# Kernel optimization log

Measured on AMD Instinct MI355X. Metric: run time of the kernel, lower is better.

Reference implementation:

```python
import jax, jax.numpy as jnp
import numpy as np

N, E, H, EA, C = 50000, 800000, 128, 32, 4
EPS = 1e-8


def _mlp(x, w1, b1, w2, b2, last_act=False):
    h = jax.nn.silu(x @ w1 + b1)
    o = h @ w2 + b2
    return jax.nn.silu(o) if last_act else o


def _seg_mean(src, idx, n):
    s = jax.ops.segment_sum(src, idx, num_segments=n)
    cnt = jax.ops.segment_sum(jnp.ones((src.shape[0], 1), src.dtype), idx, num_segments=n)
    return s / jnp.maximum(cnt, 1.0)


def setup_inputs() -> dict:
    key = jax.random.key(0)
    ks = jax.random.split(key, 24)

    def lin(k, fan_in, fan_out):
        kw, kb = jax.random.split(k)
        s = 1.0 / np.sqrt(fan_in)
        return (jax.random.uniform(kw, (fan_in, fan_out), jnp.float32, -s, s),
                jax.random.uniform(kb, (fan_out,), jnp.float32, -s, s))

    node_feat = jax.random.normal(ks[0], (N, H), jnp.float32)
    node_pos = jax.random.normal(ks[1], (N, 3), jnp.float32)
    edge_index = jax.random.randint(ks[2], (2, E), 0, N, jnp.int32)
    edge_attr = jax.random.normal(ks[3], (E, EA), jnp.float32)

    fi_w1, fi_b1 = lin(ks[4], H, H)
    fi_w2, fi_b2 = lin(ks[5], H, H)
    msg_in = 2 * H + EA + 4
    msg_w1, msg_b1 = lin(ks[6], msg_in, H)
    msg_w2, msg_b2 = lin(ks[7], H, H)
    co_w1, co_b1 = lin(ks[8], H, H)
    co_w2, co_b2 = lin(ks[9], H, C)
    vf_w1, vf_b1 = lin(ks[10], H, H)
    vf_w2, vf_b2 = lin(ks[11], H, H)

    return dict(node_feat=node_feat, node_pos=node_pos, edge_index=edge_index,
                edge_attr=edge_attr,
                fi_w1=fi_w1, fi_b1=fi_b1, fi_w2=fi_w2, fi_b2=fi_b2,
                msg_w1=msg_w1, msg_b1=msg_b1, msg_w2=msg_w2, msg_b2=msg_b2,
                co_w1=co_w1, co_b1=co_b1, co_w2=co_w2, co_b2=co_b2,
                vf_w1=vf_w1, vf_b1=vf_b1, vf_w2=vf_w2, vf_b2=vf_b2)


def reference(node_feat, node_pos, edge_index, edge_attr,
              fi_w1, fi_b1, fi_w2, fi_b2,
              msg_w1, msg_b1, msg_w2, msg_b2,
              co_w1, co_b1, co_w2, co_b2,
              vf_w1, vf_b1, vf_w2, vf_b2):
    n = node_feat.shape[0]
    # node-level init (mlp_feat_init has last_act=True)
    vn_feat = _mlp(node_feat, fi_w1, fi_b1, fi_w2, fi_b2, last_act=True)
    vn_pos = jnp.tile(node_pos, (1, C))  # [N, 3C]

    row, col = edge_index[0], edge_index[1]
    diff_pos = node_pos[row] - node_pos[col]                      # [E,3]
    nrm = jnp.maximum(jnp.linalg.norm(diff_pos, axis=-1, keepdims=True), EPS)
    diff_vec_norm = diff_pos / nrm                                # [E,3]
    dist_sq = jnp.sum(diff_pos * diff_pos, axis=-1, keepdims=True)
    ip = jnp.tile(dist_sq, (1, 4))                                # [E,4]

    msg = jnp.concatenate([node_feat[row], node_feat[col], edge_attr, ip], axis=1)
    msg = _mlp(msg, msg_w1, msg_b1, msg_w2, msg_b2)               # [E,H]

    # FullyConnectedTensorProduct 1x1o x 1x0e(=1) -> Cx1o reduces to per-channel
    # scaling of the unit vector by the learned weights (path norm factor = 1).
    w_coff = _mlp(msg, co_w1, co_b1, co_w2, co_b2)                # [E,C]
    diff_vec_out = (w_coff[:, :, None] * diff_vec_norm[:, None, :]).reshape(-1, 3 * C)

    agg_feat = _seg_mean(msg, row, n)                             # [N,H]
    agg_vec = _seg_mean(diff_vec_out, row, n)                     # [N,3C]

    vn_feat = vn_feat + _mlp(agg_feat, vf_w1, vf_b1, vf_w2, vf_b2)
    vn_pos = vn_pos + agg_vec
    return (vn_feat, vn_pos)
```

## Files before the change

kernel.cpp:

```cpp
#include <hip/hip_runtime.h>
#include <math.h>

#define N_NODES 50000
#define NTOT    50176
#define NB      196
#define N_EDGES 800000
#define H       128

typedef _Float16 f16x8 __attribute__((ext_vector_type(8)));
typedef _Float16 f16x4 __attribute__((ext_vector_type(4)));
typedef float    f32x4 __attribute__((ext_vector_type(4)));

#define KP1 320
#define KS1 10
#define KS2 4

#define XOFF 0
#define MOFF 0
#define HOFF 40960
#define XSTR 640
#define HSTR 256
#define LDSB 57344

__device__ __forceinline__ float fast_rcp(float x) {
#if __has_builtin(__builtin_amdgcn_rcpf)
    return __builtin_amdgcn_rcpf(x);
#else
    return 1.0f / x;
#endif
}
__device__ __forceinline__ float fast_exp2(float x) {
#if __has_builtin(__builtin_amdgcn_exp2f)
    return __builtin_amdgcn_exp2f(x);
#else
    return exp2f(x);
#endif
}
__device__ __forceinline__ float silu_f(float x) {
    return x * fast_rcp(1.0f + fast_exp2(-1.44269504089f * x));
}

__global__ void pack_w(const float* __restrict__ W, int K, int KP, int NCOL,
                       int CT, _Float16* __restrict__ out) {
    const int idx = blockIdx.x * 256 + threadIdx.x;
    const int KS = KP >> 5;
    if (idx >= CT * 16 * KP) return;
    const int j = idx & 7, l = (idx >> 3) & 63, rem = idx >> 9;
    const int ct = rem / KS, ks = rem % KS;
    const int k = ks * 32 + (l >> 4) * 8 + j;
    const int c = ct * 16 + (l & 15);
    out[idx] = (_Float16)((k < K && c < NCOL) ? W[k * NCOL + c] : 0.0f);
}

__global__ void k_hist(const int* __restrict__ eidx, int* __restrict__ cnt) {
    const int e = blockIdx.x * 256 + threadIdx.x;
    atomicAdd(&cnt[eidx[e]], 1);
}

__global__ void k_scan1(const int* __restrict__ cnt, int* __restrict__ offs,
                        int* __restrict__ bsum) {
    __shared__ int sd[256];
    const int t = threadIdx.x;
    const int idx = blockIdx.x * 256 + t;
    const int v = cnt[idx];
    sd[t] = v;
    __syncthreads();
    for (int off = 1; off < 256; off <<= 1) {
        int x = (t >= off) ? sd[t - off] : 0;
        __syncthreads();
        sd[t] += x;
        __syncthreads();
    }
    offs[idx] = sd[t] - v;
    if (t == 255) bsum[blockIdx.x] = sd[255];
}

__global__ void k_scan2(int* __restrict__ bsum) {
    __shared__ int sd[256];
    const int t = threadIdx.x;
    const int v = (t < NB) ? bsum[t] : 0;
    sd[t] = v;
    __syncthreads();
    for (int off = 1; off < 256; off <<= 1) {
        int x = (t >= off) ? sd[t - off] : 0;
        __syncthreads();
        sd[t] += x;
        __syncthreads();
    }
    if (t < NB) bsum[t] = sd[t] - v;
}

__global__ void k_addcur(int* __restrict__ offs, const int* __restrict__ bsum,
                         int* __restrict__ cursor) {
    const int idx = blockIdx.x * 256 + threadIdx.x;
    const int v = offs[idx] + bsum[blockIdx.x];
    offs[idx] = v;
    cursor[idx] = v;
}

__global__ void k_scatter(const int* __restrict__ eidx, int* __restrict__ cursor,
                          int* __restrict__ perm) {
    const int e = blockIdx.x * 256 + threadIdx.x;
    const int r = eidx[e];
    const int p = atomicAdd(&cursor[r], 1);
    perm[p] = e;
}

__device__ __forceinline__ f16x8 ld_frag(const char* sp, int off, int row,
                                         int strideB, int kb) {
    const int byte = (off + row * strideB + kb * 2) ^ ((row & 7) << 4);
    return *(const f16x8*)(sp + byte);
}
__device__ __forceinline__ void st_f16(char* sp, int off, int row, int col,
                                       _Float16 v) {
    const int byte = (off + row * HSTR + col * 2) ^ ((row & 7) << 4);
    *(_Float16*)(sp + byte) = v;
}
__device__ __forceinline__ float ld_f16(const char* sp, int off, int row, int col) {
    const int byte = (off + row * HSTR + col * 2) ^ ((row & 7) << 4);
    return (float)*(const _Float16*)(sp + byte);
}

#define MFMA_GEMM(OFF, STRIDEB, KS, WPK)                                      \
    {                                                                         \
        _Pragma("unroll")                                                     \
        for (int ks = 0; ks < (KS); ++ks) {                                   \
            const f16x8 b = *(const f16x8*)&(WPK)[(((w * (KS)) + ks) * 64 + lane) * 8]; \
            _Pragma("unroll")                                                 \
            for (int rt = 0; rt < 4; ++rt) {                                  \
                const f16x8 a = ld_frag(sp, (OFF), rt * 16 + lr, (STRIDEB),   \
                                        ks * 32 + lk * 8);                    \
                acc[rt] = __builtin_amdgcn_mfma_f32_16x16x32_f16(a, b, acc[rt], 0, 0, 0); \
            }                                                                 \
        }                                                                     \
    }

#define ACC_ZERO { _Pragma("unroll") for (int rt = 0; rt < 4; ++rt) acc[rt] = (f32x4)0.0f; }

#define EPILOGUE(OFF, BIAS, ACT)                                              \
    {                                                                         \
        const int col = w * 16 + lr;                                          \
        const float bv = (BIAS)[col];                                         \
        _Pragma("unroll")                                                     \
        for (int rt = 0; rt < 4; ++rt) {                                      \
            _Pragma("unroll")                                                 \
            for (int i = 0; i < 4; ++i) {                                     \
                float v = acc[rt][i] + bv;                                    \
                if (ACT) v = silu_f(v);                                       \
                st_f16(sp, (OFF), rt * 16 + lk * 4 + i, col, (_Float16)v);    \
            }                                                                 \
        }                                                                     \
    }

__global__ __launch_bounds__(512, 4) void edge_kernel(
    const float* __restrict__ feat, const float* __restrict__ pos,
    const int*   __restrict__ eidx, const float* __restrict__ eattr,
    const int*   __restrict__ perm,
    const _Float16* __restrict__ wpk1, const float* __restrict__ mb1,
    const _Float16* __restrict__ wpk2, const float* __restrict__ mb2,
    const _Float16* __restrict__ wpk3, const float* __restrict__ cb1,
    const _Float16* __restrict__ wpk4, const float* __restrict__ cb2,
    float* __restrict__ agg_msg, float* __restrict__ agg_vec)
{
    __shared__ alignas(16) char Sb[LDSB];
    __shared__ float unitS[64][3];
    __shared__ float coffS[64][4];
    __shared__ int   rowS[64];
    __shared__ int   colS[64];
    __shared__ int   peS[64];
    __shared__ int   runListS[65];
    __shared__ int   nRunsS;
    char* sp = (char*)Sb;

    const int t    = threadIdx.x;
    const int lane = t & 63;
    const int w    = t >> 6;
    const int lr   = lane & 15;
    const int lk   = lane >> 4;
    const int e0   = blockIdx.x * 64;

    if (t < 64) {
        const int pe = perm[e0 + t];
        const int r = eidx[pe];
        const int c = eidx[N_EDGES + pe];
        peS[t] = pe; rowS[t] = r; colS[t] = c;
        const float dx = pos[r*3+0] - pos[c*3+0];
        const float dy = pos[r*3+1] - pos[c*3+1];
        const float dz = pos[r*3+2] - pos[c*3+2];
        const float dsq = dx*dx + dy*dy + dz*dz;
        const float inv = 1.0f / fmaxf(sqrtf(dsq), 1e-8f);
        unitS[t][0] = dx * inv;
        unitS[t][1] = dy * inv;
        unitS[t][2] = dz * inv;
        const int prev = __shfl_up(r, 1);
        const bool isStart = (t == 0) || (prev != r);
        const unsigned long long mask = __ballot(isStart);
        const int nR = __popcll(mask);
        if (isStart) runListS[__popcll(mask & ((1ull << t) - 1))] = t;
        if (t == 0)  nRunsS = nR;
        if (t == 63) runListS[nR] = 64;
        f16x8 dv = (f16x8)(_Float16)0.0f;
        const _Float16 dh = (_Float16)dsq;
        dv[0] = dh; dv[1] = dh; dv[2] = dh; dv[3] = dh;
        const int byte = (XOFF + t * XSTR + 288 * 2) ^ ((t & 7) << 4);
        *(f16x8*)(sp + byte) = dv;
    }
    if (t < 256) {
        const int e = t >> 2, c = t & 3;
        if (c < 3) {
            const int byte = (XOFF + e * XSTR + (296 + c * 8) * 2) ^ ((e & 7) << 4);
            *(f16x8*)(sp + byte) = (f16x8)(_Float16)0.0f;
        }
    }
    __syncthreads();

    const float4* feat4 = (const float4*)feat;
    #pragma unroll
    for (int s = 0; s < 8; ++s) {
        const int flat = t + 512 * s;
        const int e = flat >> 6, rest = flat & 63;
        const int side = rest >> 5, q = rest & 31;
        const int node = side ? colS[e] : rowS[e];
        const float4 v = feat4[(size_t)node * 32 + q];
        f16x4 o; o[0]=(_Float16)v.x; o[1]=(_Float16)v.y; o[2]=(_Float16)v.z; o[3]=(_Float16)v.w;
        const int byte = (XOFF + e * XSTR + (side * 128 + q * 4) * 2) ^ ((e & 7) << 4);
        *(f16x4*)(sp + byte) = o;
    }
    {
        const int e = t >> 3, q = t & 7;
        const float4 v = ((const float4*)eattr)[(size_t)peS[e] * 8 + q];
        f16x4 o; o[0]=(_Float16)v.x; o[1]=(_Float16)v.y; o[2]=(_Float16)v.z; o[3]=(_Float16)v.w;
        const int byte = (XOFF + e * XSTR + (256 + q * 4) * 2) ^ ((e & 7) << 4);
        *(f16x4*)(sp + byte) = o;
    }
    __syncthreads();

    f32x4 acc[4];

    ACC_ZERO
    MFMA_GEMM(XOFF, XSTR, KS1, wpk1)
    EPILOGUE(HOFF, mb1, 1)
    __syncthreads();

    ACC_ZERO
    MFMA_GEMM(HOFF, HSTR, KS2, wpk2)
    EPILOGUE(MOFF, mb2, 0)
    __syncthreads();

    ACC_ZERO
    MFMA_GEMM(MOFF, HSTR, KS2, wpk3)
    EPILOGUE(HOFF, cb1, 1)
    __syncthreads();

    if (w < 4) {
        f32x4 a4 = (f32x4)0.0f;
        #pragma unroll
        for (int ks = 0; ks < 4; ++ks) {
            const f16x8 b = *(const f16x8*)&wpk4[(ks * 64 + lane) * 8];
            const f16x8 a = ld_frag(sp, HOFF, w * 16 + lr, HSTR, ks * 32 + lk * 8);
            a4 = __builtin_amdgcn_mfma_f32_16x16x32_f16(a, b, a4, 0, 0, 0);
        }
        if (lr < 4) {
            #pragma unroll
            for (int i = 0; i < 4; ++i)
                coffS[w * 16 + lk * 4 + i][lr] = a4[i] + cb2[lr];
        }
    }

    const int nR = nRunsS;
    for (int it = t; it < nR * 128; it += 512) {
        const int run = it >> 7, c = it & 127;
        const int s = runListS[run], epos = runListS[run + 1];
        float a = 0.0f;
        for (int k = s; k < epos; ++k) a += ld_f16(sp, MOFF, k, c);
        atomicAdd(&agg_msg[(size_t)rowS[s] * H + c], a);
    }
    __syncthreads();

    for (int it = t; it < nR * 12; it += 512) {
        const int run = it / 12, m = it % 12;
        const int s = runListS[run], epos = runListS[run + 1];
        float a = 0.0f;
        for (int k = s; k < epos; ++k) a += coffS[k][m / 3] * unitS[k][m % 3];
        atomicAdd(&agg_vec[(size_t)rowS[s] * 12 + m], a);
    }
}

#define AOFF 0
#define BOFF 16384
#define NLDS 32768

__global__ __launch_bounds__(512, 4) void node_kernel(
    const float* __restrict__ feat, const float* __restrict__ pos,
    const _Float16* __restrict__ wf1, const float* __restrict__ fb1,
    const _Float16* __restrict__ wf2, const float* __restrict__ fb2,
    const _Float16* __restrict__ wv1, const float* __restrict__ vb1,
    const _Float16* __restrict__ wv2, const float* __restrict__ vb2,
    const float* __restrict__ agg_msg, const float* __restrict__ agg_vec,
    const int* __restrict__ cnt_i, float* __restrict__ out)
{
    __shared__ alignas(16) char Sb[NLDS];
    __shared__ float invS[64];
    char* sp = (char*)Sb;

    const int t    = threadIdx.x;
    const int lane = t & 63;
    const int w    = t >> 6;
    const int lr   = lane & 15;
    const int lk   = lane >> 4;
    const int n0   = blockIdx.x * 64;

    const float4* feat4 = (const float4*)feat;
    #pragma unroll
    for (int s = 0; s < 4; ++s) {
        const int flat = t + 512 * s;
        const int e = flat >> 5, q = flat & 31;
        const int node = n0 + e;
        float4 v = make_float4(0.f, 0.f, 0.f, 0.f);
        if (node < N_NODES) v = feat4[(size_t)node * 32 + q];
        f16x4 o; o[0]=(_Float16)v.x; o[1]=(_Float16)v.y; o[2]=(_Float16)v.z; o[3]=(_Float16)v.w;
        const int byte = (AOFF + e * HSTR + q * 8) ^ ((e & 7) << 4);
        *(f16x4*)(sp + byte) = o;
    }
    if (t < 64) {
        const int node = n0 + t;
        const float c = (node < N_NODES) ? (float)cnt_i[node] : 1.0f;
        invS[t] = fast_rcp(fmaxf(c, 1.0f));
    }
    __syncthreads();

    f32x4 acc[4];
    float resid[4][4];

    ACC_ZERO
    MFMA_GEMM(AOFF, HSTR, KS2, wf1)
    EPILOGUE(BOFF, fb1, 1)
    __syncthreads();

    ACC_ZERO
    MFMA_GEMM(BOFF, HSTR, KS2, wf2)
    {
        const float bv = fb2[w * 16 + lr];
        #pragma unroll
        for (int rt = 0; rt < 4; ++rt)
            #pragma unroll
            for (int i = 0; i < 4; ++i)
                resid[rt][i] = silu_f(acc[rt][i] + bv);
    }
    __syncthreads();

    const float4* agg4 = (const float4*)agg_msg;
    #pragma unroll
    for (int s = 0; s < 4; ++s) {
        const int flat = t + 512 * s;
        const int e = flat >> 5, q = flat & 31;
        const int node = n0 + e;
        float4 v = make_float4(0.f, 0.f, 0.f, 0.f);
        if (node < N_NODES) v = agg4[(size_t)node * 32 + q];
        const float iv = invS[e];
        f16x4 o; o[0]=(_Float16)(v.x*iv); o[1]=(_Float16)(v.y*iv);
        o[2]=(_Float16)(v.z*iv); o[3]=(_Float16)(v.w*iv);
        const int byte = (AOFF + e * HSTR + q * 8) ^ ((e & 7) << 4);
        *(f16x4*)(sp + byte) = o;
    }
    __syncthreads();

    ACC_ZERO
    MFMA_GEMM(AOFF, HSTR, KS2, wv1)
    EPILOGUE(BOFF, vb1, 1)
    __syncthreads();

    ACC_ZERO
    MFMA_GEMM(BOFF, HSTR, KS2, wv2)
    {
        const int col = w * 16 + lr;
        const float bv = vb2[col];
        #pragma unroll
        for (int rt = 0; rt < 4; ++rt) {
            #pragma unroll
            for (int i = 0; i < 4; ++i) {
                const int node = n0 + rt * 16 + lk * 4 + i;
                if (node < N_NODES)
                    out[(size_t)node * H + col] = acc[rt][i] + bv + resid[rt][i];
            }
        }
    }

    for (int fl = t; fl < 64 * 12; fl += 512) {
        const int e = fl / 12, m = fl % 12;
        const int node = n0 + e;
        if (node < N_NODES)
            out[(size_t)N_NODES * H + (size_t)node * 12 + m] =
                pos[node * 3 + (m % 3)] + agg_vec[(size_t)node * 12 + m] * invS[e];
    }
}

extern "C" void kernel_launch(void* const* d_in, const int* in_sizes, int n_in,
                              void* d_out, int out_size, void* d_ws, size_t ws_size,
                              hipStream_t stream)
{
    const float* node_feat = (const float*)d_in[0];
    const float* node_pos  = (const float*)d_in[1];
    const int*   eidx      = (const int*)  d_in[2];
    const float* eattr     = (const float*)d_in[3];
    const float* fi_w1  = (const float*)d_in[4];
    const float* fi_b1  = (const float*)d_in[5];
    const float* fi_w2  = (const float*)d_in[6];
    const float* fi_b2  = (const float*)d_in[7];
    const float* msg_w1 = (const float*)d_in[8];
    const float* msg_b1 = (const float*)d_in[9];
    const float* msg_w2 = (const float*)d_in[10];
    const float* msg_b2 = (const float*)d_in[11];
    const float* co_w1  = (const float*)d_in[12];
    const float* co_b1  = (const float*)d_in[13];
    const float* co_w2  = (const float*)d_in[14];
    const float* co_b2  = (const float*)d_in[15];
    const float* vf_w1  = (const float*)d_in[16];
    const float* vf_b1  = (const float*)d_in[17];
    const float* vf_w2  = (const float*)d_in[18];
    const float* vf_b2  = (const float*)d_in[19];

    float* out     = (float*)d_out;
    float* agg_msg = (float*)d_ws;
    float* agg_vec = agg_msg + (size_t)N_NODES * H;
    int*   cnt_i   = (int*)(agg_vec + (size_t)N_NODES * 12);
    int*   offs    = cnt_i + NTOT;
    int*   cursor  = offs + NTOT;
    int*   bsum    = cursor + NTOT;
    int*   perm    = bsum + 256;
    _Float16* wpk1 = (_Float16*)(perm + N_EDGES);
    _Float16* wpk2 = wpk1 + 128 * KP1;
    _Float16* wpk3 = wpk2 + 128 * 128;
    _Float16* wpk4 = wpk3 + 128 * 128;
    _Float16* wpkF1 = wpk4 + 16 * 128;
    _Float16* wpkF2 = wpkF1 + 128 * 128;
    _Float16* wpkV1 = wpkF2 + 128 * 128;
    _Float16* wpkV2 = wpkV1 + 128 * 128;

    hipMemsetAsync(d_ws, 0,
                   ((size_t)N_NODES * (H + 12) + NTOT) * sizeof(float), stream);

    pack_w<<<(8 * 16 * KP1 + 255) / 256, 256, 0, stream>>>(msg_w1, 292, KP1, 128, 8, wpk1);
    pack_w<<<(8 * 16 * 128 + 255) / 256, 256, 0, stream>>>(msg_w2, 128, 128, 128, 8, wpk2);
    pack_w<<<(8 * 16 * 128 + 255) / 256, 256, 0, stream>>>(co_w1, 128, 128, 128, 8, wpk3);
    pack_w<<<(1 * 16 * 128 + 255) / 256, 256, 0, stream>>>(co_w2, 128, 128, 4, 1, wpk4);
    pack_w<<<(8 * 16 * 128 + 255) / 256, 256, 0, stream>>>(fi_w1, 128, 128, 128, 8, wpkF1);
    pack_w<<<(8 * 16 * 128 + 255) / 256, 256, 0, stream>>>(fi_w2, 128, 128, 128, 8, wpkF2);
    pack_w<<<(8 * 16 * 128 + 255) / 256, 256, 0, stream>>>(vf_w1, 128, 128, 128, 8, wpkV1);
    pack_w<<<(8 * 16 * 128 + 255) / 256, 256, 0, stream>>>(vf_w2, 128, 128, 128, 8, wpkV2);

    k_hist<<<N_EDGES / 256, 256, 0, stream>>>(eidx, cnt_i);
    k_scan1<<<NB, 256, 0, stream>>>(cnt_i, offs, bsum);
    k_scan2<<<1, 256, 0, stream>>>(bsum);
    k_addcur<<<NB, 256, 0, stream>>>(offs, bsum, cursor);
    k_scatter<<<N_EDGES / 256, 256, 0, stream>>>(eidx, cursor, perm);

    edge_kernel<<<N_EDGES / 64, 512, 0, stream>>>(
        node_feat, node_pos, eidx, eattr, perm,
        wpk1, msg_b1, wpk2, msg_b2, wpk3, co_b1, wpk4, co_b2,
        agg_msg, agg_vec);

    node_kernel<<<(N_NODES + 63) / 64, 512, 0, stream>>>(
        node_feat, node_pos,
        wpkF1, fi_b1, wpkF2, fi_b2, wpkV1, vf_b1, wpkV2, vf_b2,
        agg_msg, agg_vec, cnt_i, out);
}
```

Before: 644.3 us.

## Precompute per-node first-layer projections and reduce edge GEMM to edge-attr part

Result: no change. 641.2 us (-0.5%).

```diff
diff --git a/kernel.cpp b/kernel.cpp
--- a/kernel.cpp
+++ b/kernel.cpp
@@ -11,16 +11,14 @@
 typedef _Float16 f16x4 __attribute__((ext_vector_type(4)));
 typedef float    f32x4 __attribute__((ext_vector_type(4)));
 
-#define KP1 320
-#define KS1 10
 #define KS2 4
 
-#define XOFF 0
-#define MOFF 0
-#define HOFF 40960
-#define XSTR 640
-#define HSTR 256
-#define LDSB 57344
+#define GOFF  0
+#define MOFF  0
+#define HOFF2 16384
+#define EAOFF 32768
+#define HSTR  256
+#define LDSB  36864
 
 __device__ __forceinline__ float fast_rcp(float x) {
 #if __has_builtin(__builtin_amdgcn_rcpf)
@@ -40,16 +38,40 @@
     return x * fast_rcp(1.0f + fast_exp2(-1.44269504089f * x));
 }
 
-__global__ void pack_w(const float* __restrict__ W, int K, int KP, int NCOL,
-                       int CT, _Float16* __restrict__ out) {
-    const int idx = blockIdx.x * 256 + threadIdx.x;
+__device__ __forceinline__ void pack_one(const float* __restrict__ W, int K,
+                                         int KP, int NCOL,
+                                         _Float16* __restrict__ out, int idx) {
     const int KS = KP >> 5;
-    if (idx >= CT * 16 * KP) return;
     const int j = idx & 7, l = (idx >> 3) & 63, rem = idx >> 9;
     const int ct = rem / KS, ks = rem % KS;
     const int k = ks * 32 + (l >> 4) * 8 + j;
     const int c = ct * 16 + (l & 15);
     out[idx] = (_Float16)((k < K && c < NCOL) ? W[k * NCOL + c] : 0.0f);
+}
+
+__global__ void pack_all(const float* __restrict__ msg_w1, const float* __restrict__ msg_w2,
+                         const float* __restrict__ co_w1, const float* __restrict__ co_w2,
+                         const float* __restrict__ fi_w1, const float* __restrict__ fi_w2,
+                         const float* __restrict__ vf_w1, const float* __restrict__ vf_w2,
+                         _Float16* __restrict__ wR, _Float16* __restrict__ wC,
+                         _Float16* __restrict__ wEA, _Float16* __restrict__ w2,
+                         _Float16* __restrict__ w3, _Float16* __restrict__ w4,
+                         _Float16* __restrict__ wF1, _Float16* __restrict__ wF2,
+                         _Float16* __restrict__ wV1, _Float16* __restrict__ wV2,
+                         float* __restrict__ wip) {
+    const int b = blockIdx.x, t = threadIdx.x;
+    if      (b < 64)  pack_one(msg_w1,             128, 128, 128, wR,  b * 256 + t);
+    else if (b < 128) pack_one(msg_w1 + 128 * 128, 128, 128, 128, wC,  (b - 64) * 256 + t);
+    else if (b < 144) pack_one(msg_w1 + 256 * 128, 32,  32,  128, wEA, (b - 128) * 256 + t);
+    else if (b < 208) pack_one(msg_w2, 128, 128, 128, w2,  (b - 144) * 256 + t);
+    else if (b < 272) pack_one(co_w1,  128, 128, 128, w3,  (b - 208) * 256 + t);
+    else if (b < 280) pack_one(co_w2,  128, 128, 4,   w4,  (b - 272) * 256 + t);
+    else if (b < 344) pack_one(fi_w1,  128, 128, 128, wF1, (b - 280) * 256 + t);
+    else if (b < 408) pack_one(fi_w2,  128, 128, 128, wF2, (b - 344) * 256 + t);
+    else if (b < 472) pack_one(vf_w1,  128, 128, 128, wV1, (b - 408) * 256 + t);
+    else if (b < 536) pack_one(vf_w2,  128, 128, 128, wV2, (b - 472) * 256 + t);
+    else if (t < 128) wip[t] = msg_w1[288 * 128 + t] + msg_w1[289 * 128 + t]
+                             + msg_w1[290 * 128 + t] + msg_w1[291 * 128 + t];
 }
 
 __global__ void k_hist(const int* __restrict__ eidx, int* __restrict__ cnt) {
@@ -101,8 +123,7 @@
 __global__ void k_scatter(const int* __restrict__ eidx, int* __restrict__ cursor,
                           int* __restrict__ perm) {
     const int e = blockIdx.x * 256 + threadIdx.x;
-    const int r = eidx[e];
-    const int p = atomicAdd(&cursor[r], 1);
+    const int p = atomicAdd(&cursor[eidx[e]], 1);
     perm[p] = e;
 }
 
@@ -152,11 +173,63 @@
         }                                                                     \
     }
 
-__global__ __launch_bounds__(512, 4) void edge_kernel(
-    const float* __restrict__ feat, const float* __restrict__ pos,
-    const int*   __restrict__ eidx, const float* __restrict__ eattr,
-    const int*   __restrict__ perm,
-    const _Float16* __restrict__ wpk1, const float* __restrict__ mb1,
+__global__ __launch_bounds__(512, 4) void prc_kernel(
+    const float* __restrict__ feat,
+    const _Float16* __restrict__ wR, const _Float16* __restrict__ wC,
+    _Float16* __restrict__ pr16, _Float16* __restrict__ pc16)
+{
+    __shared__ alignas(16) char Sb[16384];
+    char* sp = (char*)Sb;
+    const int t = threadIdx.x;
+    const int lane = t & 63, w = t >> 6;
+    const int lr = lane & 15, lk = lane >> 4;
+    const int n0 = blockIdx.x * 64;
+
+    const float4* feat4 = (const float4*)feat;
+    #pragma unroll
+    for (int s = 0; s < 4; ++s) {
+        const int flat = t + 512 * s;
+        const int e = flat >> 5, q = flat & 31;
+        const int node = n0 + e;
+        float4 v = make_float4(0.f, 0.f, 0.f, 0.f);
+        if (node < N_NODES) v = feat4[(size_t)node * 32 + q];
+        f16x4 o; o[0]=(_Float16)v.x; o[1]=(_Float16)v.y; o[2]=(_Float16)v.z; o[3]=(_Float16)v.w;
+        const int byte = (e * HSTR + q * 8) ^ ((e & 7) << 4);
+        *(f16x4*)(sp + byte) = o;
+    }
+    __syncthreads();
+
+    f32x4 acc[4];
+    const int col = w * 16 + lr;
+
+    ACC_ZERO
+    MFMA_GEMM(0, HSTR, KS2, wR)
+    #pragma unroll
+    for (int rt = 0; rt < 4; ++rt)
+        #pragma unroll
+        for (int i = 0; i < 4; ++i) {
+            const int node = n0 + rt * 16 + lk * 4 + i;
+            if (node < N_NODES) pr16[(size_t)node * H + col] = (_Float16)acc[rt][i];
+        }
+
+    ACC_ZERO
+    MFMA_GEMM(0, HSTR, KS2, wC)
+    #pragma unroll
+    for (int rt = 0; rt < 4; ++rt)
+        #pragma unroll
+        for (int i = 0; i < 4; ++i) {
+            const int node = n0 + rt * 16 + lk * 4 + i;
+            if (node < N_NODES) pc16[(size_t)node * H + col] = (_Float16)acc[rt][i];
+        }
+}
+
+__global__ __launch_bounds__(512, 8) void edge_kernel(
+    const _Float16* __restrict__ pr16, const _Float16* __restrict__ pc16,
+    const float* __restrict__ pos,
+    const int* __restrict__ eidx, const float* __restrict__ eattr,
+    const int* __restrict__ perm,
+    const _Float16* __restrict__ wEA, const float* __restrict__ wip,
+    const float* __restrict__ mb1,
     const _Float16* __restrict__ wpk2, const float* __restrict__ mb2,
     const _Float16* __restrict__ wpk3, const float* __restrict__ cb1,
     const _Float16* __restrict__ wpk4, const float* __restrict__ cb2,
@@ -165,6 +238,7 @@
     __shared__ alignas(16) char Sb[LDSB];
     __shared__ float unitS[64][3];
     __shared__ float coffS[64][4];
+    __shared__ float dsqS[64];
     __shared__ int   rowS[64];
     __shared__ int   colS[64];
     __shared__ int   peS[64];
@@ -192,6 +266,7 @@
         unitS[t][0] = dx * inv;
         unitS[t][1] = dy * inv;
         unitS[t][2] = dz * inv;
+        dsqS[t] = dsq;
         const int prev = __shfl_up(r, 1);
         const bool isStart = (t == 0) || (prev != r);
         const unsigned long long mask = __ballot(isStart);
@@ -199,57 +274,61 @@
         if (isStart) runListS[__popcll(mask & ((1ull << t) - 1))] = t;
         if (t == 0)  nRunsS = nR;
         if (t == 63) runListS[nR] = 64;
-        f16x8 dv = (f16x8)(_Float16)0.0f;
-        const _Float16 dh = (_Float16)dsq;
-        dv[0] = dh; dv[1] = dh; dv[2] = dh; dv[3] = dh;
-        const int byte = (XOFF + t * XSTR + 288 * 2) ^ ((t & 7) << 4);
-        *(f16x8*)(sp + byte) = dv;
-    }
-    if (t < 256) {
-        const int e = t >> 2, c = t & 3;
-        if (c < 3) {
-            const int byte = (XOFF + e * XSTR + (296 + c * 8) * 2) ^ ((e & 7) << 4);
-            *(f16x8*)(sp + byte) = (f16x8)(_Float16)0.0f;
-        }
-    }
-    __syncthreads();
-
-    const float4* feat4 = (const float4*)feat;
+    }
+    __syncthreads();
+
     #pragma unroll
-    for (int s = 0; s < 8; ++s) {
+    for (int s = 0; s < 2; ++s) {
         const int flat = t + 512 * s;
-        const int e = flat >> 6, rest = flat & 63;
-        const int side = rest >> 5, q = rest & 31;
-        const int node = side ? colS[e] : rowS[e];
-        const float4 v = feat4[(size_t)node * 32 + q];
-        f16x4 o; o[0]=(_Float16)v.x; o[1]=(_Float16)v.y; o[2]=(_Float16)v.z; o[3]=(_Float16)v.w;
-        const int byte = (XOFF + e * XSTR + (side * 128 + q * 4) * 2) ^ ((e & 7) << 4);
-        *(f16x4*)(sp + byte) = o;
+        const int e = flat >> 4, q = flat & 15;
+        const f16x8 a = *(const f16x8*)&pr16[(size_t)rowS[e] * H + q * 8];
+        const f16x8 b = *(const f16x8*)&pc16[(size_t)colS[e] * H + q * 8];
+        const f16x8 g = a + b;
+        const int byte = (GOFF + e * HSTR + q * 16) ^ ((e & 7) << 4);
+        *(f16x8*)(sp + byte) = g;
     }
     {
         const int e = t >> 3, q = t & 7;
         const float4 v = ((const float4*)eattr)[(size_t)peS[e] * 8 + q];
         f16x4 o; o[0]=(_Float16)v.x; o[1]=(_Float16)v.y; o[2]=(_Float16)v.z; o[3]=(_Float16)v.w;
-        const int byte = (XOFF + e * XSTR + (256 + q * 4) * 2) ^ ((e & 7) << 4);
-        *(f16x4*)(sp + byte) = o;
+        *(f16x4*)(sp + EAOFF + e * 64 + q * 8) = o;
     }
     __syncthreads();
 
     f32x4 acc[4];
-
-    ACC_ZERO
-    MFMA_GEMM(XOFF, XSTR, KS1, wpk1)
-    EPILOGUE(HOFF, mb1, 1)
-    __syncthreads();
-
-    ACC_ZERO
-    MFMA_GEMM(HOFF, HSTR, KS2, wpk2)
+    const int col = w * 16 + lr;
+
+    ACC_ZERO
+    {
+        const f16x8 bEA = *(const f16x8*)&wEA[(w * 64 + lane) * 8];
+        #pragma unroll
+        for (int rt = 0; rt < 4; ++rt) {
+            const f16x8 a = *(const f16x8*)(sp + EAOFF + (rt * 16 + lr) * 64 + lk * 16);
+            acc[rt] = __builtin_amdgcn_mfma_f32_16x16x32_f16(a, bEA, acc[rt], 0, 0, 0);
+        }
+    }
+    {
+        const float bv = mb1[col];
+        const float wipv = wip[col];
+        #pragma unroll
+        for (int rt = 0; rt < 4; ++rt)
+            #pragma unroll
+            for (int i = 0; i < 4; ++i) {
+                const int row = rt * 16 + lk * 4 + i;
+                float v = acc[rt][i] + bv + dsqS[row] * wipv + ld_f16(sp, GOFF, row, col);
+                st_f16(sp, HOFF2, row, col, (_Float16)silu_f(v));
+            }
+    }
+    __syncthreads();
+
+    ACC_ZERO
+    MFMA_GEMM(HOFF2, HSTR, KS2, wpk2)
     EPILOGUE(MOFF, mb2, 0)
     __syncthreads();
 
     ACC_ZERO
     MFMA_GEMM(MOFF, HSTR, KS2, wpk3)
-    EPILOGUE(HOFF, cb1, 1)
+    EPILOGUE(HOFF2, cb1, 1)
     __syncthreads();
 
     if (w < 4) {
@@ -257,7 +336,7 @@
         #pragma unroll
         for (int ks = 0; ks < 4; ++ks) {
             const f16x8 b = *(const f16x8*)&wpk4[(ks * 64 + lane) * 8];
-            const f16x8 a = ld_frag(sp, HOFF, w * 16 + lr, HSTR, ks * 32 + lk * 8);
+            const f16x8 a = ld_frag(sp, HOFF2, w * 16 + lr, HSTR, ks * 32 + lk * 8);
             a4 = __builtin_amdgcn_mfma_f32_16x16x32_f16(a, b, a4, 0, 0, 0);
         }
         if (lr < 4) {
@@ -265,23 +344,30 @@
             for (int i = 0; i < 4; ++i)
                 coffS[w * 16 + lk * 4 + i][lr] = a4[i] + cb2[lr];
         }
-    }
+    } else {
+        const int nR = nRunsS;
+        for (int it = t - 256; it < nR * 16; it += 256) {
+            const int run = it >> 4, q = it & 15;
+            const int s = runListS[run], e1 = runListS[run + 1];
+            float a[8] = {0.f, 0.f, 0.f, 0.f, 0.f, 0.f, 0.f, 0.f};
+            for (int k = s; k < e1; ++k) {
+                const f16x8 v = ld_frag(sp, MOFF, k, HSTR, q * 8);
+                #pragma unroll
+                for (int j = 0; j < 8; ++j) a[j] += (float)v[j];
+            }
+            float* dst = &agg_msg[(size_t)rowS[s] * H + q * 8];
+            #pragma unroll
+            for (int j = 0; j < 8; ++j) atomicAdd(&dst[j], a[j]);
+        }
+    }
+    __syncthreads();
 
     const int nR = nRunsS;
-    for (int it = t; it < nR * 128; it += 512) {
-        const int run = it >> 7, c = it & 127;
-        const int s = runListS[run], epos = runListS[run + 1];
-        float a = 0.0f;
-        for (int k = s; k < epos; ++k) a += ld_f16(sp, MOFF, k, c);
-        atomicAdd(&agg_msg[(size_t)rowS[s] * H + c], a);
-    }
-    __syncthreads();
-
     for (int it = t; it < nR * 12; it += 512) {
         const int run = it / 12, m = it % 12;
-        const int s = runListS[run], epos = runListS[run + 1];
+        const int s = runListS[run], e1 = runListS[run + 1];
         float a = 0.0f;
-        for (int k = s; k < epos; ++k) a += coffS[k][m / 3] * unitS[k][m % 3];
+        for (int k = s; k < e1; ++k) a += coffS[k][m / 3] * unitS[k][m % 3];
         atomicAdd(&agg_vec[(size_t)rowS[s] * 12 + m], a);
     }
 }
@@ -428,26 +514,27 @@
     int*   cursor  = offs + NTOT;
     int*   bsum    = cursor + NTOT;
     int*   perm    = bsum + 256;
-    _Float16* wpk1 = (_Float16*)(perm + N_EDGES);
-    _Float16* wpk2 = wpk1 + 128 * KP1;
-    _Float16* wpk3 = wpk2 + 128 * 128;
-    _Float16* wpk4 = wpk3 + 128 * 128;
-    _Float16* wpkF1 = wpk4 + 16 * 128;
-    _Float16* wpkF2 = wpkF1 + 128 * 128;
-    _Float16* wpkV1 = wpkF2 + 128 * 128;
-    _Float16* wpkV2 = wpkV1 + 128 * 128;
+    _Float16* pr16 = (_Float16*)(perm + N_EDGES);
+    _Float16* pc16 = pr16 + (size_t)N_NODES * H;
+    _Float16* wR   = pc16 + (size_t)N_NODES * H;
+    _Float16* wC   = wR + 16384;
+    _Float16* wEA  = wC + 16384;
+    _Float16* wpk2 = wEA + 4096;
+    _Float16* wpk3 = wpk2 + 16384;
+    _Float16* wpk4 = wpk3 + 16384;
+    _Float16* wF1  = wpk4 + 2048;
+    _Float16* wF2  = wF1 + 16384;
+    _Float16* wV1  = wF2 + 16384;
+    _Float16* wV2  = wV1 + 16384;
+    float*    wip  = (float*)(wV2 + 16384);
 
     hipMemsetAsync(d_ws, 0,
                    ((size_t)N_NODES * (H + 12) + NTOT) * sizeof(float), stream);
 
-    pack_w<<<(8 * 16 * KP1 + 255) / 256, 256, 0, stream>>>(msg_w1, 292, KP1, 128, 8, wpk1);
-    pack_w<<<(8 * 16 * 128 + 255) / 256, 256, 0, stream>>>(msg_w2, 128, 128, 128, 8, wpk2);
-    pack_w<<<(8 * 16 * 128 + 255) / 256, 256, 0, stream>>>(co_w1, 128, 128, 128, 8, wpk3);
-    pack_w<<<(1 * 16 * 128 + 255) / 256, 256, 0, stream>>>(co_w2, 128, 128, 4, 1, wpk4);
-    pack_w<<<(8 * 16 * 128 + 255) / 256, 256, 0, stream>>>(fi_w1, 128, 128, 128, 8, wpkF1);
-    pack_w<<<(8 * 16 * 128 + 255) / 256, 256, 0, stream>>>(fi_w2, 128, 128, 128, 8, wpkF2);
-    pack_w<<<(8 * 16 * 128 + 255) / 256, 256, 0, stream>>>(vf_w1, 128, 128, 128, 8, wpkV1);
-    pack_w<<<(8 * 16 * 128 + 255) / 256, 256, 0, stream>>>(vf_w2, 128, 128, 128, 8, wpkV2);
+    pack_all<<<537, 256, 0, stream>>>(msg_w1, msg_w2, co_w1, co_w2,
+                                      fi_w1, fi_w2, vf_w1, vf_w2,
+                                      wR, wC, wEA, wpk2, wpk3, wpk4,
+                                      wF1, wF2, wV1, wV2, wip);
 
     k_hist<<<N_EDGES / 256, 256, 0, stream>>>(eidx, cnt_i);
     k_scan1<<<NB, 256, 0, stream>>>(cnt_i, offs, bsum);
@@ -455,13 +542,15 @@
     k_addcur<<<NB, 256, 0, stream>>>(offs, bsum, cursor);
     k_scatter<<<N_EDGES / 256, 256, 0, stream>>>(eidx, cursor, perm);
 
+    prc_kernel<<<(N_NODES + 63) / 64, 512, 0, stream>>>(node_feat, wR, wC, pr16, pc16);
+
     edge_kernel<<<N_EDGES / 64, 512, 0, stream>>>(
-        node_feat, node_pos, eidx, eattr, perm,
-        wpk1, msg_b1, wpk2, msg_b2, wpk3, co_b1, wpk4, co_b2,
+        pr16, pc16, node_pos, eidx, eattr, perm,
+        wEA, wip, msg_b1, wpk2, msg_b2, wpk3, co_b1, wpk4, co_b2,
         agg_msg, agg_vec);
 
     node_kernel<<<(N_NODES + 63) / 64, 512, 0, stream>>>(
         node_feat, node_pos,
-        wpkF1, fi_b1, wpkF2, fi_b2, wpkV1, vf_b1, wpkV2, vf_b2,
+        wF1, fi_b1, wF2, fi_b2, wV1, vf_b1, wV2, vf_b2,
         agg_msg, agg_vec, cnt_i, out);
 }
```
